# Performance work log

Hardware: AMD Instinct MI355X
Metric: run time of the kernel (lower is better)

Reference implementation:

```python
import jax, jax.numpy as jnp
import numpy as np

# sarModule stage: in=256, out=512, blocks=2, stride=2, patch_groups=4, mask_size=7
B, C_IN, H, W = 32, 256, 56, 56
C_OUT = 512
PLANES = C_OUT // 4   # Bottleneck inner width = planes // expansion = 128
G = 4                 # patch_groups
MS = 7                # mask_size
TEMP = 1.0            # gumbel-softmax temperature


def conv(x, w, stride=1, pad=0, groups=1):
    return jax.lax.conv_general_dilated(
        x, w, (stride, stride), [(pad, pad), (pad, pad)],
        feature_group_count=groups,
        dimension_numbers=('NCHW', 'OIHW', 'NCHW'))


def bn(x, g, b):
    # BatchNorm in inference form with running_mean=0, running_var=1 folded in
    return x * g[None, :, None, None] + b[None, :, None, None]


def avgpool3s2(x):
    # nn.AvgPool2d(3, stride=2, padding=1), count_include_pad=True
    s = jax.lax.reduce_window(x, 0.0, jax.lax.add, (1, 1, 3, 3), (1, 1, 2, 2),
                              [(0, 0), (0, 0), (1, 1), (1, 1)])
    return s / 9.0


def setup_inputs() -> dict:
    key = jax.random.key(0)
    ks = iter(jax.random.split(key, 64))

    def w(shape):
        fan_in = int(np.prod(shape[1:]))
        return jax.random.normal(next(ks), shape, jnp.float32) * np.float32((2.0 / fan_in) ** 0.5)

    ones = lambda n: jnp.ones((n,), jnp.float32)
    zeros = lambda n: jnp.zeros((n,), jnp.float32)

    x = jax.random.normal(next(ks), (B, C_IN, H, W), jnp.float32)
    u = jax.random.uniform(next(ks), (B, 2, G, MS, MS), jnp.float32, 1e-6, 1.0 - 1e-6)
    gumbel_noise = -jnp.log(-jnp.log(u))

    return dict(
        x=x, gumbel_noise=gumbel_noise,
        # base Bottleneck (256->512, stride 2, downsample = avgpool + 1x1 conv + bn)
        b_w1=w((PLANES, C_IN, 1, 1)), b_g1=ones(PLANES), b_b1=zeros(PLANES),
        b_w2=w((PLANES, PLANES, 3, 3)), b_g2=ones(PLANES), b_b2=zeros(PLANES),
        b_w3=w((C_OUT, PLANES, 1, 1)), b_g3=ones(C_OUT), b_b3=zeros(C_OUT),
        b_dw=w((C_OUT, C_IN, 1, 1)), b_dg=ones(C_OUT), b_db=zeros(C_OUT),
        # refine Bottleneck (256->512, stride 1, downsample = 1x1 conv + bn)
        r_w1=w((PLANES, C_IN, 1, 1)), r_g1=ones(PLANES), r_b1=zeros(PLANES),
        r_w2=w((PLANES, PLANES, 3, 3)), r_g2=ones(PLANES), r_b2=zeros(PLANES),
        r_w3=w((C_OUT, PLANES, 1, 1)), r_g3=ones(C_OUT), r_b3=zeros(C_OUT),
        r_dw=w((C_OUT, C_IN, 1, 1)), r_dg=ones(C_OUT), r_db=zeros(C_OUT),
        # maskGen: grouped 3x3 conv (512 -> 4*G), bn, pool, grouped 1x1 fc (4*G -> 2*G)
        m_w=w((4 * G, C_OUT // G, 3, 3)), m_g=ones(4 * G), m_b=zeros(4 * G),
        m_fcw=w((2 * G, 4, 1, 1)),
        m_fcb=jnp.concatenate([0.1 * ones(G), 5.0 * ones(G)]),  # bias init from maskGen
        # fusion Bottleneck (512->512, stride 2, downsample = avgpool only)
        f_w1=w((PLANES, C_OUT, 1, 1)), f_g1=ones(PLANES), f_b1=zeros(PLANES),
        f_w2=w((PLANES, PLANES, 3, 3)), f_g2=ones(PLANES), f_b2=zeros(PLANES),
        f_w3=w((C_OUT, PLANES, 1, 1)), f_g3=ones(C_OUT), f_b3=zeros(C_OUT),
    )


def reference(x, gumbel_noise,
              b_w1, b_g1, b_b1, b_w2, b_g2, b_b2, b_w3, b_g3, b_b3, b_dw, b_dg, b_db,
              r_w1, r_g1, r_b1, r_w2, r_g2, r_b2, r_w3, r_g3, r_b3, r_dw, r_dg, r_db,
              m_w, m_g, m_b, m_fcw, m_fcb,
              f_w1, f_g1, f_b1, f_w2, f_g2, f_b2, f_w3, f_g3, f_b3):
    # ---- base branch: Bottleneck stride 2, last_relu=False -> [B,512,28,28]
    o = jax.nn.relu(bn(conv(x, b_w1), b_g1, b_b1))
    o = jax.nn.relu(bn(conv(o, b_w2, stride=2, pad=1), b_g2, b_b2))
    o = bn(conv(o, b_w3), b_g3, b_b3)
    x_base = o + bn(conv(avgpool3s2(x), b_dw), b_dg, b_db)

    # ---- maskGen on x_base
    gmap = jax.nn.relu(bn(conv(x_base, m_w, pad=1, groups=G), m_g, m_b))      # [B,16,28,28]
    hb = x_base.shape[2] // MS                                                 # adaptive avgpool 28->7
    gmap = gmap.reshape(B, 4 * G, MS, hb, MS, hb).mean(axis=(3, 5))            # [B,16,7,7]
    logits = conv(gmap, m_fcw, groups=G) + m_fcb[None, :, None, None]          # [B,8,7,7]
    logits = logits.reshape(B, 2, G, MS, MS)                                   # view(B,2,groups,ms,ms)
    # hard gumbel-softmax over dim 1 with straight-through estimator
    y = jax.nn.softmax((logits + gumbel_noise) / TEMP, axis=1)
    hard = jax.nn.one_hot(jnp.argmax(y, axis=1), 2, axis=1, dtype=y.dtype)
    gates = hard + y - jax.lax.stop_gradient(y)
    mask = gates[:, 1]                                                         # [B,G,7,7]

    # nearest-upsample mask x8 and expand across each channel group
    mask_up = jnp.repeat(jnp.repeat(mask, H // MS, axis=-2), W // MS, axis=-1) # [B,G,56,56]
    mask_full = jnp.broadcast_to(mask_up[:, :, None], (B, G, C_OUT // G, H, W)).reshape(B, C_OUT, H, W)

    # ---- refine branch: Bottleneck stride 1, output gated by mask, last_relu=False
    o = jax.nn.relu(bn(conv(x, r_w1), r_g1, r_b1))
    o = jax.nn.relu(bn(conv(o, r_w2, pad=1), r_g2, r_b2))
    o = bn(conv(o, r_w3), r_g3, r_b3) * mask_full
    x_refine = o + bn(conv(x, r_dw), r_dg, r_db)                               # [B,512,56,56]

    # ---- fuse: bilinear upsample base to refine resolution (align_corners=False)
    x_base_up = jax.image.resize(x_base, (B, C_OUT, H, W), 'bilinear')
    fused = jax.nn.relu(x_base_up + x_refine)

    # ---- fusion Bottleneck: stride 2, downsample = avgpool only, last_relu=True
    o = jax.nn.relu(bn(conv(fused, f_w1), f_g1, f_b1))
    o = jax.nn.relu(bn(conv(o, f_w2, stride=2, pad=1), f_g2, f_b2))
    o = bn(conv(o, f_w3), f_g3, f_b3)
    out = jax.nn.relu(o + avgpool3s2(fused))                                   # [B,512,28,28]
    return out, mask
```

## Files before the change

### kernel.cpp

```cpp
#include <hip/hip_runtime.h>
#include <cstdint>

#define BB   32
#define CINX 256
#define HH   56
#define WW   56
#define HWX  3136
#define CO   512
#define PL   128
#define HP   28
#define WP   28
#define HWP  784
#define NG   4
#define MSZ  7

typedef unsigned short ushortT;
typedef unsigned int   uint32;
typedef __attribute__((ext_vector_type(8))) short short8;
typedef __attribute__((ext_vector_type(4))) float f32x4;

__device__ __forceinline__ ushortT f2bf(float f){
  uint32 u = __float_as_uint(f);
  u = (u + 0x7fffu + ((u >> 16) & 1u)) >> 16;
  return (ushortT)u;
}
__device__ __forceinline__ float bf2f(ushortT u){
  return __uint_as_float(((uint32)u) << 16);
}
__device__ __forceinline__ void split2(float v, ushortT& h, ushortT& lo){
  h = f2bf(v);
  lo = f2bf(v - bf2f(h));
}
__device__ __forceinline__ uint32 packu(ushortT a, ushortT b){
  return (uint32)a | ((uint32)b << 16);
}

typedef __attribute__((address_space(1))) const void g_void;
typedef __attribute__((address_space(3))) void l_void;
__device__ __forceinline__ void glds16(const ushortT* g, ushortT* l){
  __builtin_amdgcn_global_load_lds((g_void*)g, (l_void*)l, 16, 0, 0);
}

__device__ __forceinline__ void wsplit(float v, ushortT* dh, ushortT* dl, size_t i){
  ushortT h, lo; split2(v, h, lo); dh[i] = h; dl[i] = lo;
}

__global__ __launch_bounds__(256) void prep_w(
  const float* __restrict__ b_w1, const float* __restrict__ b_g1,
  const float* __restrict__ b_w2, const float* __restrict__ b_g2,
  const float* __restrict__ b_w3, const float* __restrict__ b_g3,
  const float* __restrict__ b_dw, const float* __restrict__ b_dg,
  const float* __restrict__ r_w1, const float* __restrict__ r_g1,
  const float* __restrict__ r_w2, const float* __restrict__ r_g2,
  const float* __restrict__ r_w3, const float* __restrict__ r_g3,
  const float* __restrict__ r_dw, const float* __restrict__ r_dg,
  const float* __restrict__ f_w1, const float* __restrict__ f_g1,
  const float* __restrict__ f_w2, const float* __restrict__ f_g2,
  const float* __restrict__ f_w3, const float* __restrict__ f_g3,
  const float* __restrict__ b_b1, const float* __restrict__ r_b1,
  ushortT* __restrict__ dh, ushortT* __restrict__ dl,
  ushortT* __restrict__ zp, float* __restrict__ biasC)
{
  const int idx = blockIdx.x*256 + threadIdx.x;
  switch (blockIdx.y){
    case 0: {
      if (idx >= 32768) return; int m = idx >> 8;
      wsplit(b_w1[idx]*b_g1[m], dh, dl, (size_t)0 + idx); } break;
    case 3: {
      if (idx >= 32768) return; int m = idx >> 8;
      wsplit(r_w1[idx]*r_g1[m], dh, dl, 32768 + (size_t)idx); } break;
    case 1: {
      if (idx >= 147456) return; int m = idx / 1152; int k = idx - m*1152;
      int tap = k >> 7, c = k & 127;
      wsplit(b_w2[((size_t)(m*128 + c))*9 + tap]*b_g2[m], dh, dl, 65536 + (size_t)idx); } break;
    case 2: {
      if (idx >= 196608) return; int m = idx / 384; int k = idx - m*384;
      float v = (k < 128) ? b_w3[m*128 + k]*b_g3[m] : b_dw[m*256 + (k-128)]*b_dg[m];
      wsplit(v, dh, dl, 212992 + (size_t)idx); } break;
    case 4: {
      if (idx >= 147456) return; int m = idx / 1152; int k = idx - m*1152;
      int tap = k >> 7, c = k & 127;
      wsplit(r_w2[((size_t)(m*128 + c))*9 + tap]*r_g2[m], dh, dl, 409600 + (size_t)idx); } break;
    case 5: {
      if (idx >= 196608) return; int m = idx / 384; int k = idx - m*384;
      float v = (k < 128) ? r_w3[m*128 + k]*r_g3[m] : r_dw[m*256 + (k-128)]*r_dg[m];
      wsplit(v, dh, dl, 557056 + (size_t)idx); } break;
    case 6: {
      if (idx >= 65536) return; int m = idx >> 9;
      wsplit(f_w1[idx]*f_g1[m], dh, dl, 753664 + (size_t)idx); } break;
    case 7: {
      if (idx >= 147456) return; int m = idx / 1152; int k = idx - m*1152;
      int tap = k >> 7, c = k & 127;
      wsplit(f_w2[((size_t)(m*128 + c))*9 + tap]*f_g2[m], dh, dl, 819200 + (size_t)idx); } break;
    case 8: {
      if (idx >= 65536) return; int m = idx >> 7;
      wsplit(f_w3[idx]*f_g3[m], dh, dl, 966656 + (size_t)idx); } break;
    case 9: {
      if (idx < 64) zp[idx] = 0;
      if (idx < 128) biasC[idx] = b_b1[idx];
      else if (idx < 256) biasC[idx] = r_b1[idx-128];
    } break;
  }
}

__global__ __launch_bounds__(256) void k_avgpool_x(const float* __restrict__ x, float* __restrict__ out){
  int idx = blockIdx.x*256 + threadIdx.x;
  if (idx >= BB*CINX*HWP) return;
  int p = idx % HWP; int bc = idx / HWP;
  int ox = p % WP, oy = p / WP;
  const float* src = x + (size_t)bc*HWX;
  float s = 0.f;
  #pragma unroll
  for (int dy=0; dy<3; dy++){
    int yy = 2*oy-1+dy;
    if ((unsigned)yy >= HH) continue;
    #pragma unroll
    for (int dx=0; dx<3; dx++){
      int xx = 2*ox-1+dx;
      if ((unsigned)xx >= WW) continue;
      s += src[yy*WW + xx];
    }
  }
  out[idx] = s * (1.f/9.f);
}

__global__ __launch_bounds__(256) void prep_p(const float* __restrict__ t,
    ushortT* __restrict__ ph_, ushortT* __restrict__ pl_){
  __shared__ float s[16][17];
  const int p0 = blockIdx.x*16, c0 = blockIdx.y*16, bz = blockIdx.z;
  const int ci = threadIdx.x >> 4, pi = threadIdx.x & 15;
  s[ci][pi] = t[((size_t)bz*CINX + c0 + ci)*HWP + p0 + pi];
  __syncthreads();
  const int pr = threadIdx.x >> 4, cj = threadIdx.x & 15;
  float v = s[cj][pr];
  ushortT h, lo; split2(v, h, lo);
  size_t o = ((size_t)bz*HWP + p0 + pr)*CINX + c0 + cj;
  ph_[o] = h; pl_[o] = lo;
}

__global__ __launch_bounds__(256) void prep_x2(const float* __restrict__ x,
    ushortT* __restrict__ xh, ushortT* __restrict__ xl){
  __shared__ float s[16][17];
  const int p0 = blockIdx.x*16, c0 = blockIdx.y*16, bz = blockIdx.z;
  const int ci = threadIdx.x >> 4, pi = threadIdx.x & 15;
  s[ci][pi] = x[((size_t)bz*CINX + c0 + ci)*HWX + p0 + pi];
  __syncthreads();
  const int pr = threadIdx.x >> 4, cj = threadIdx.x & 15;
  float v = s[cj][pr];
  ushortT h, lo; split2(v, h, lo);
  size_t o = ((size_t)bz*HWX + p0 + pr)*CINX + c0 + cj;
  xh[o] = h; xl[o] = lo;
}

__global__ __launch_bounds__(256) void k_poolf(const ushortT* __restrict__ fzh,
    const ushortT* __restrict__ fzl, float* __restrict__ pf){
  const int p = blockIdx.x, bz = blockIdx.y;
  const int oy = p / WP, ox = p - oy*WP;
  const int c = threadIdx.x*2;
  float s0 = 0.f, s1 = 0.f;
  #pragma unroll
  for (int dy=0; dy<3; dy++){
    const int iy = 2*oy - 1 + dy;
    if ((unsigned)iy >= (unsigned)HH) continue;
    #pragma unroll
    for (int dx=0; dx<3; dx++){
      const int ix = 2*ox - 1 + dx;
      if ((unsigned)ix >= (unsigned)WW) continue;
      const size_t fi = ((size_t)bz*HWX + (size_t)(iy*WW + ix))*CO + c;
      uint32 hh = *(const uint32*)(fzh + fi);
      uint32 ll = *(const uint32*)(fzl + fi);
      s0 += bf2f((ushortT)(hh & 0xffff)) + bf2f((ushortT)(ll & 0xffff));
      s1 += bf2f((ushortT)(hh >> 16))    + bf2f((ushortT)(ll >> 16));
    }
  }
  const size_t o = ((size_t)bz*HWP + p)*CO + c;
  pf[o]   = s0 * (1.f/9.f);
  pf[o+1] = s1 * (1.f/9.f);
}

template<int KIND,int EPI,int S1F,int MT,int DBUF,int SWAP,int STRIDE,int PAD,
         int HIN,int WIN,int WOUT,int NOUT,int C1,int C2,int BSTR1,int MTOT,int KTOT>
__global__ __launch_bounds__(MT*2)
void gemm_bf3(const ushortT* __restrict__ wph, const ushortT* __restrict__ wpl,
              const ushortT* __restrict__ s1h, const ushortT* __restrict__ s1l,
              const ushortT* __restrict__ s2h, const ushortT* __restrict__ s2l,
              const float* __restrict__ xf32,
              const float* __restrict__ bias1, const float* __restrict__ bias2,
              const float* __restrict__ maskf, const float* __restrict__ xbase,
              const ushortT* __restrict__ zp,
              ushortT* __restrict__ oh, ushortT* __restrict__ ol,
              float* __restrict__ of32)
{
  constexpr int NW = MT/32;
  constexpr int BCALLS = 8/NW;
  constexpr bool GATHER1 = (KIND==0 && S1F==1);
  constexpr int BUFSZ = MT*64 + 8192;
  __shared__ ushortT smem[BUFSZ*(DBUF+1)];

  const int tid = threadIdx.x;
  const int nt = SWAP ? blockIdx.y : blockIdx.x;
  const int mt = SWAP ? blockIdx.x : blockIdx.y;
  const int bz = blockIdx.z;
  const int l  = tid & 63, w = tid >> 6;
  const int wm = w >> 1, wn = w & 1;

  size_t a_src[2]; int a_dst[2];
  #pragma unroll
  for (int c=0;c<2;c++){
    int s = (w*2 + c)*64 + l;
    int row = s >> 2, slotm = s & 3;
    int logical = slotm ^ ((row >> 1) & 3);
    a_src[c] = (size_t)(mt*MT + row)*KTOT + logical*8;
    a_dst[c] = (w*2 + c)*512;
  }

  int b_dst[2]; size_t b_base1[2], b_base2[2]; int b_klane[2];
  int b_oy[2], b_ox[2]; bool b_ok[2]; float b_mv[2];
  #pragma unroll
  for (int c=0;c<BCALLS;c++){
    int s = (w*BCALLS + c)*64 + l;
    int row = s >> 2, slotm = s & 3;
    int logical = slotm ^ ((row >> 1) & 3);
    b_klane[c] = logical*8;
    b_dst[c] = (w*BCALLS + c)*512;
    int ngr = nt*128 + row;
    b_ok[c] = (ngr < NOUT);
    int oyv = ngr / WOUT, oxv = ngr - (ngr / WOUT)*WOUT;
    b_oy[c] = oyv; b_ox[c] = oxv;
    b_base1[c] = ((size_t)bz*NOUT + ngr)*BSTR1 + b_klane[c];
    b_base2[c] = ((size_t)bz*NOUT + ngr)*C2 + b_klane[c];
    b_mv[c] = 1.f;
    if (KIND == 3)
      b_mv[c] = b_ok[c] ? maskf[((size_t)(bz*NG + mt)*MSZ + (oyv>>3))*MSZ + (oxv>>3)] : 0.f;
  }

  const int sr = tid >> 1;
  const int hp = tid & 1;
  const int swz = (sr >> 1) & 3;
  const int lws0 = sr*32 + ((2*hp) ^ swz)*8;
  const int lws1 = sr*32 + ((2*hp + 1) ^ swz)*8;
  const int ng = nt*128 + sr;

  f32x4 acc[4][4];
  f32x4 zf = {0.f,0.f,0.f,0.f};
  #pragma unroll
  for (int i=0;i<4;i++)
    #pragma unroll
    for (int j=0;j<4;j++) acc[i][j] = zf;

  auto stagef = [&](int ks, ushortT* AHb, ushortT* ALb, ushortT* BHb, ushortT* BLb){
    const int k0 = ks*32;
    #pragma unroll
    for (int c=0;c<2;c++){
      glds16(wph + a_src[c] + k0, AHb + a_dst[c]);
      glds16(wpl + a_src[c] + k0, ALb + a_dst[c]);
    }
    if constexpr (GATHER1){
      if (tid < 256){
        uint4 b0 = make_uint4(0,0,0,0), b1v = b0, b2v = b0, b3v = b0;
        if (ng < NOUT){
          size_t fbase = ((size_t)bz*C1 + k0 + hp*16)*(size_t)NOUT + ng;
          ushortT h[16], lo[16];
          #pragma unroll
          for (int e=0;e<16;e++){ split2(xf32[fbase + (size_t)e*NOUT], h[e], lo[e]); }
          b0  = make_uint4(packu(h[0],h[1]),  packu(h[2],h[3]),  packu(h[4],h[5]),  packu(h[6],h[7]));
          b1v = make_uint4(packu(h[8],h[9]),  packu(h[10],h[11]),packu(h[12],h[13]),packu(h[14],h[15]));
          b2v = make_uint4(packu(lo[0],lo[1]),packu(lo[2],lo[3]),packu(lo[4],lo[5]),packu(lo[6],lo[7]));
          b3v = make_uint4(packu(lo[8],lo[9]),packu(lo[10],lo[11]),packu(lo[12],lo[13]),packu(lo[14],lo[15]));
        }
        *(uint4*)(BHb + lws0) = b0;  *(uint4*)(BHb + lws1) = b1v;
        *(uint4*)(BLb + lws0) = b2v; *(uint4*)(BLb + lws1) = b3v;
      }
    } else {
      #pragma unroll
      for (int c=0;c<BCALLS;c++){
        const ushortT *sh, *sl;
        if constexpr (KIND == 0){
          bool ok = b_ok[c];
          size_t off = b_base1[c] + k0;
          sh = ok ? s1h + off : zp;  sl = ok ? s1l + off : zp;
        } else if constexpr (KIND == 1){
          const int tap = k0 >> 7;
          const int cb  = (k0 & 127);
          const int dy = tap/3, dx = tap - 3*(tap/3);
          int iy = b_oy[c]*STRIDE + dy - PAD;
          int ix = b_ox[c]*STRIDE + dx - PAD;
          bool ok = b_ok[c] && (unsigned)iy < (unsigned)HIN && (unsigned)ix < (unsigned)WIN;
          size_t off = ((size_t)bz*(HIN*WIN) + (size_t)(iy*WIN + ix))*BSTR1 + cb + b_klane[c];
          sh = ok ? s1h + off : zp;  sl = ok ? s1l + off : zp;
        } else {
          if (k0 < C1){
            bool ok = b_ok[c] && (KIND != 3 || b_mv[c] != 0.f);
            size_t off = b_base1[c] + k0;
            sh = ok ? s1h + off : zp;  sl = ok ? s1l + off : zp;
          } else {
            bool ok = b_ok[c];
            size_t off = b_base2[c] + (k0 - C1);
            sh = ok ? s2h + off : zp;  sl = ok ? s2l + off : zp;
          }
        }
        glds16(sh, BHb + b_dst[c]);
        glds16(sl, BLb + b_dst[c]);
      }
    }
  };

  auto computef = [&](const ushortT* AHb, const ushortT* ALb,
                      const ushortT* BHb, const ushortT* BLb){
    short8 bh[4], bl[4];
    #pragma unroll
    for (int nf=0; nf<4; nf++){
      const int rr = wn*64 + nf*16 + (l & 15);
      const int ph = (l >> 4) ^ ((rr >> 1) & 3);
      bh[nf] = *(const short8*)(BHb + rr*32 + ph*8);
      bl[nf] = *(const short8*)(BLb + rr*32 + ph*8);
    }
    #pragma unroll
    for (int mf=0; mf<4; mf++){
      const int rr = wm*64 + mf*16 + (l & 15);
      const int ph = (l >> 4) ^ ((rr >> 1) & 3);
      short8 ah = *(const short8*)(AHb + rr*32 + ph*8);
      short8 al = *(const short8*)(ALb + rr*32 + ph*8);
      #pragma unroll
      for (int nf=0; nf<4; nf++)
        acc[mf][nf] = __builtin_amdgcn_mfma_f32_16x16x32_bf16(ah, bh[nf], acc[mf][nf], 0,0,0);
      #pragma unroll
      for (int nf=0; nf<4; nf++)
        acc[mf][nf] = __builtin_amdgcn_mfma_f32_16x16x32_bf16(ah, bl[nf], acc[mf][nf], 0,0,0);
      #pragma unroll
      for (int nf=0; nf<4; nf++)
        acc[mf][nf] = __builtin_amdgcn_mfma_f32_16x16x32_bf16(al, bh[nf], acc[mf][nf], 0,0,0);
    }
  };

  const int NK = KTOT / 32;
  if constexpr (DBUF == 0){
    ushortT* AH  = smem;
    ushortT* AL  = smem + MT*32;
    ushortT* BHs = smem + MT*64;
    ushortT* BLs = smem + MT*64 + 4096;
    for (int ks=0; ks<NK; ks++){
      stagef(ks, AH, AL, BHs, BLs);
      __syncthreads();
      computef(AH, AL, BHs, BLs);
      __syncthreads();
    }
  } else {
    stagef(0, smem, smem + MT*32, smem + MT*64, smem + MT*64 + 4096);
    __syncthreads();
    for (int ks=0; ks<NK; ks++){
      ushortT* cb = smem + (ks & 1)*BUFSZ;
      ushortT* nb = smem + ((ks & 1) ^ 1)*BUFSZ;
      if (ks + 1 < NK)
        stagef(ks + 1, nb, nb + MT*32, nb + MT*64, nb + MT*64 + 4096);
      computef(cb, cb + MT*32, cb + MT*64, cb + MT*64 + 4096);
      __syncthreads();
    }
  }

  const int mb0 = mt*MT + wm*64;
  const int nb0 = nt*128 + wn*64;

  #pragma unroll
  for (int nf=0; nf<4; nf++){
    const int n = nb0 + nf*16 + (l & 15);
    if (n >= NOUT) continue;
    if constexpr (EPI == 0){
      const size_t ob = ((size_t)bz*NOUT + n)*MTOT;
      #pragma unroll
      for (int mf=0; mf<4; mf++){
        const int m0 = mb0 + mf*16 + (l>>4)*4;
        ushort4 hq, lq; ushortT h0, l0; float v;
        v = fmaxf(acc[mf][nf][0] + bias1[m0+0], 0.f); split2(v,h0,l0); hq.x=h0; lq.x=l0;
        v = fmaxf(acc[mf][nf][1] + bias1[m0+1], 0.f); split2(v,h0,l0); hq.y=h0; lq.y=l0;
        v = fmaxf(acc[mf][nf][2] + bias1[m0+2], 0.f); split2(v,h0,l0); hq.z=h0; lq.z=l0;
        v = fmaxf(acc[mf][nf][3] + bias1[m0+3], 0.f); split2(v,h0,l0); hq.w=h0; lq.w=l0;
        *(ushort4*)(oh + ob + m0) = hq;
        *(ushort4*)(ol + ob + m0) = lq;
      }
    } else if constexpr (EPI == 1){
      #pragma unroll
      for (int mf=0; mf<4; mf++){
        const int m0 = mb0 + mf*16 + (l>>4)*4;
        #pragma unroll
        for (int r=0;r<4;r++){
          const int m = m0 + r;
          of32[((size_t)bz*MTOT + m)*NOUT + n] = acc[mf][nf][r] + bias1[m] + bias2[m];
        }
      }
    } else if constexpr (EPI == 2){
      const int y = n / WOUT, x = n - (n / WOUT)*WOUT;
      const int grpw = (mt*MT + wm*64) >> 7;
      const float mvv = maskf[((size_t)(bz*NG + grpw)*MSZ + (y>>3))*MSZ + (x>>3)];
      const int iy = y >> 1, ix = x >> 1;
      int yA,yB,xA,xB; float wyA,wyB,wxA,wxB;
      if (y & 1){ yA=iy; wyA=0.75f; yB=(iy+1<HP)?iy+1:HP-1; wyB=0.25f; }
      else      { yA=(iy>0)?iy-1:0; wyA=0.25f; yB=iy; wyB=0.75f; }
      if (x & 1){ xA=ix; wxA=0.75f; xB=(ix+1<WP)?ix+1:WP-1; wxB=0.25f; }
      else      { xA=(ix>0)?ix-1:0; wxA=0.25f; xB=ix; wxB=0.75f; }
      const size_t ob = ((size_t)bz*NOUT + n)*MTOT;
      #pragma unroll
      for (int mf=0; mf<4; mf++){
        const int m0 = mb0 + mf*16 + (l>>4)*4;
        ushort4 hq, lq;
        #pragma unroll
        for (int r=0;r<4;r++){
          const int m = m0 + r;
          const float* xb = xbase + ((size_t)bz*MTOT + m)*HWP;
          float up = wyA*(wxA*xb[yA*WP+xA] + wxB*xb[yA*WP+xB])
                   + wyB*(wxA*xb[yB*WP+xA] + wxB*xb[yB*WP+xB]);
          float v = fmaxf(acc[mf][nf][r] + up + mvv*bias1[m] + bias2[m], 0.f);
          ushortT h0, l0; split2(v, h0, l0);
          if      (r==0){hq.x=h0;lq.x=l0;}
          else if (r==1){hq.y=h0;lq.y=l0;}
          else if (r==2){hq.z=h0;lq.z=l0;}
          else          {hq.w=h0;lq.w=l0;}
        }
        *(ushort4*)(oh + ob + m0) = hq;
        *(ushort4*)(ol + ob + m0) = lq;
      }
    } else {
      const float* pfrow = xbase + ((size_t)bz*NOUT + n)*MTOT;
      #pragma unroll
      for (int mf=0; mf<4; mf++){
        const int m0 = mb0 + mf*16 + (l>>4)*4;
        const float4 pv = *(const float4*)(pfrow + m0);
        of32[((size_t)bz*MTOT + m0+0)*NOUT + n] = fmaxf(acc[mf][nf][0] + bias1[m0+0] + pv.x, 0.f);
        of32[((size_t)bz*MTOT + m0+1)*NOUT + n] = fmaxf(acc[mf][nf][1] + bias1[m0+1] + pv.y, 0.f);
        of32[((size_t)bz*MTOT + m0+2)*NOUT + n] = fmaxf(acc[mf][nf][2] + bias1[m0+2] + pv.z, 0.f);
        of32[((size_t)bz*MTOT + m0+3)*NOUT + n] = fmaxf(acc[mf][nf][3] + bias1[m0+3] + pv.w, 0.f);
      }
    }
  }
}

#define GM_LDSW 9216
__global__ __launch_bounds__(256) void k_gmap2(const float* __restrict__ xbase,
    const float* __restrict__ mw, const float* __restrict__ mg, const float* __restrict__ mb,
    float* __restrict__ gmap){
  __shared__ float wsh[GM_LDSW];
  __shared__ float red[16][2][4][16];
  const int tile = blockIdx.x, b = blockIdx.y;
  const int tid = threadIdx.x;
  const int pl = tid & 15, cs = tid >> 4;
  const int p = tile*16 + pl;
  const int oy = p / WP, ox = p - oy*WP;
  int toff[9];
  #pragma unroll
  for (int tap=0; tap<9; tap++){
    int dy = tap/3, dx = tap - 3*dy;
    int yy = oy + dy - 1, xx = ox + dx - 1;
    toff[tap] = ((unsigned)yy < (unsigned)HP && (unsigned)xx < (unsigned)WP) ? (yy*WP + xx) : -1;
  }
  float acc[2][4] = {{0.f,0.f,0.f,0.f},{0.f,0.f,0.f,0.f}};
  for (int pass=0; pass<2; pass++){
    __syncthreads();
    for (int i = tid; i < GM_LDSW; i += 256){
      int ocl = i & 3, tap = (i >> 2) % 9, c_rel = i / 36;
      int cg = pass*256 + c_rel;
      int g = cg >> 7;
      int oc = g*4 + ocl;
      wsh[i] = mw[((size_t)(oc*128 + (cg & 127)))*9 + tap] * mg[oc];
    }
    __syncthreads();
    const float* xb = xbase + ((size_t)b*CO + pass*256 + cs*16)*HWP;
    for (int cl=0; cl<16; cl++){
      const float* xc = xb + (size_t)cl*HWP;
      const float* wr = &wsh[(cs*16 + cl)*36];
      #pragma unroll
      for (int tap=0; tap<9; tap++){
        if (toff[tap] < 0) continue;
        float v = xc[toff[tap]];
        f32x4 w4 = *(const f32x4*)(wr + tap*4);
        acc[pass][0] += v*w4[0];
        acc[pass][1] += v*w4[1];
        acc[pass][2] += v*w4[2];
        acc[pass][3] += v*w4[3];
      }
    }
  }
  #pragma unroll
  for (int pp=0; pp<2; pp++)
    #pragma unroll
    for (int o=0; o<4; o++)
      red[cs][pp][o][pl] = acc[pp][o];
  __syncthreads();
  const int oc = tid >> 4;
  const int g = oc >> 2, ocl = oc & 3, pg = g >> 1, cs0 = (g & 1)*8;
  float s = 0.f;
  #pragma unroll
  for (int t=0; t<8; t++) s += red[cs0 + t][pg][ocl][pl];
  s = fmaxf(s + mb[oc], 0.f);
  gmap[((size_t)b*16 + oc)*HWP + p] = s;
}

__global__ __launch_bounds__(256) void k_gpool(const float* __restrict__ gmap, float* __restrict__ gpool){
  int idx = blockIdx.x*256 + threadIdx.x;
  if (idx >= BB*16*49) return;
  int q = idx % 49; int t = idx / 49; int ch = t % 16; int b = t / 16;
  int my = q/7, mx = q%7;
  const float* src = gmap + ((size_t)b*16 + ch)*HWP;
  float s = 0.f;
  #pragma unroll
  for (int yb=0;yb<4;yb++)
    #pragma unroll
    for (int xb=0;xb<4;xb++)
      s += src[(my*4+yb)*WP + (mx*4+xb)];
  gpool[idx] = s * (1.f/16.f);
}

__global__ __launch_bounds__(256) void k_mask(const float* __restrict__ gpool, const float* __restrict__ fcw,
    const float* __restrict__ fcb, const float* __restrict__ gum,
    float* __restrict__ maskf, float* __restrict__ mout){
  int idx = blockIdx.x*256 + threadIdx.x;
  if (idx >= BB*NG*49) return;
  int q = idx % 49; int t = idx / 49; int g = t % NG; int b = t / NG;
  float lgt[2];
  #pragma unroll
  for (int cls=0; cls<2; cls++){
    int c = cls*NG + g;
    int gc = c >> 1;
    float s = fcb[c];
    #pragma unroll
    for (int k=0;k<4;k++)
      s += fcw[c*4+k] * gpool[((size_t)b*16 + gc*4 + k)*49 + q];
    s += gum[(((size_t)b*2 + cls)*NG + g)*49 + q];
    lgt[cls] = s;
  }
  float m = (lgt[1] > lgt[0]) ? 1.f : 0.f;
  maskf[idx] = m;
  mout[idx] = m;
}

extern "C" void kernel_launch(void* const* d_in, const int* in_sizes, int n_in,
                              void* d_out, int out_size, void* d_ws, size_t ws_size,
                              hipStream_t stream){
  const float* x    = (const float*)d_in[0];
  const float* gum  = (const float*)d_in[1];
  const float* b_w1 = (const float*)d_in[2];
  const float* b_g1 = (const float*)d_in[3];
  const float* b_b1 = (const float*)d_in[4];
  const float* b_w2 = (const float*)d_in[5];
  const float* b_g2 = (const float*)d_in[6];
  const float* b_b2 = (const float*)d_in[7];
  const float* b_w3 = (const float*)d_in[8];
  const float* b_g3 = (const float*)d_in[9];
  const float* b_b3 = (const float*)d_in[10];
  const float* b_dw = (const float*)d_in[11];
  const float* b_dg = (const float*)d_in[12];
  const float* b_db = (const float*)d_in[13];
  const float* r_w1 = (const float*)d_in[14];
  const float* r_g1 = (const float*)d_in[15];
  const float* r_b1 = (const float*)d_in[16];
  const float* r_w2 = (const float*)d_in[17];
  const float* r_g2 = (const float*)d_in[18];
  const float* r_b2 = (const float*)d_in[19];
  const float* r_w3 = (const float*)d_in[20];
  const float* r_g3 = (const float*)d_in[21];
  const float* r_b3 = (const float*)d_in[22];
  const float* r_dw = (const float*)d_in[23];
  const float* r_dg = (const float*)d_in[24];
  const float* r_db = (const float*)d_in[25];
  const float* m_w  = (const float*)d_in[26];
  const float* m_g  = (const float*)d_in[27];
  const float* m_b  = (const float*)d_in[28];
  const float* m_fcw= (const float*)d_in[29];
  const float* m_fcb= (const float*)d_in[30];
  const float* f_w1 = (const float*)d_in[31];
  const float* f_g1 = (const float*)d_in[32];
  const float* f_b1 = (const float*)d_in[33];
  const float* f_w2 = (const float*)d_in[34];
  const float* f_g2 = (const float*)d_in[35];
  const float* f_b2 = (const float*)d_in[36];
  const float* f_w3 = (const float*)d_in[37];
  const float* f_g3 = (const float*)d_in[38];
  const float* f_b3 = (const float*)d_in[39];

  char* ws = (char*)d_ws;
  constexpr size_t O_WPH  = 0;
  constexpr size_t O_WPL  = 2064384;
  constexpr size_t O_CH   = 4128768;
  constexpr size_t O_DH   = 55508992;
  constexpr size_t O_DL   = 61931520;
  constexpr size_t O_EH   = 68354048;
  constexpr size_t O_EL   = 94044160;
  constexpr size_t O_PF   = O_EH;
  constexpr size_t O_XB   = 119734272;
  constexpr size_t O_GMAP = 171114496;
  constexpr size_t O_GPOOL= 172720128;
  constexpr size_t O_MASK = 172820480;
  constexpr size_t O_FH   = 172845568;
  constexpr size_t O_PH   = 172845568;
  constexpr size_t O_PL   = 185690624;
  constexpr size_t O_FL   = 275606016;
  constexpr size_t O_ZP   = 378366464;
  constexpr size_t O_BIASC= 378366592;

  ushortT* WPH = (ushortT*)(ws + O_WPH);
  ushortT* WPL = (ushortT*)(ws + O_WPL);
  ushortT* MGH = (ushortT*)(ws + O_CH);
  ushortT* XH  = (ushortT*)(ws + O_CH);
  ushortT* F1H = (ushortT*)(ws + O_CH);
  ushortT* F1L = (ushortT*)(ws + O_CH + 25690112);
  ushortT* DHp = (ushortT*)(ws + O_DH);
  ushortT* DLp = (ushortT*)(ws + O_DL);
  ushortT* EHp = (ushortT*)(ws + O_EH);
  ushortT* ELp = (ushortT*)(ws + O_EL);
  float*   PF  = (float*)(ws + O_PF);
  float*   XB  = (float*)(ws + O_XB);
  float*   PTMP= (float*)(ws + O_XB);
  ushortT* PHp = (ushortT*)(ws + O_PH);
  ushortT* PLp = (ushortT*)(ws + O_PL);
  ushortT* FHp = (ushortT*)(ws + O_FH);
  ushortT* FLp = (ushortT*)(ws + O_FL);
  float*   GMAP = (float*)(ws + O_GMAP);
  float*   GPOOL= (float*)(ws + O_GPOOL);
  float*   MASKF= (float*)(ws + O_MASK);
  ushortT* ZP  = (ushortT*)(ws + O_ZP);
  float*   BIASC = (float*)(ws + O_BIASC);
  (void)ws_size;

  float* outp = (float*)d_out;
  float* mout = outp + (size_t)BB*CO*HWP;
  ushortT* dout_u = (ushortT*)d_out;

  dim3 blk(256), blk2(512);
  const ushortT* nu = nullptr; const float* nf_ = nullptr;
  ushortT* nuo = nullptr; float* nfo = nullptr;

  prep_w<<<dim3(768, 10), blk, 0, stream>>>(b_w1,b_g1,b_w2,b_g2,b_w3,b_g3,b_dw,b_dg,
      r_w1,r_g1,r_w2,r_g2,r_w3,r_g3,r_dw,r_dg,f_w1,f_g1,f_w2,f_g2,f_w3,f_g3,
      b_b1, r_b1, WPH, WPL, ZP, BIASC);
  k_avgpool_x<<<dim3((BB*CINX*HWP+255)/256), blk, 0, stream>>>(x, PTMP);
  prep_p<<<dim3(49, 16, BB), blk, 0, stream>>>(PTMP, PHp, PLp);

  gemm_bf3<0,0,1,256,0,0, 1,0,56,56,56,3136, 256,0,256, 256,256><<<dim3(25,1,BB), blk2, 0, stream>>>(
      WPH+0, WPL+0, nu, nu, nu, nu, x, BIASC, nf_, nf_, nf_, ZP, MGH, dout_u, nfo);
  gemm_bf3<1,0,0,128,1,0, 2,1,56,56,28,784, 128,0,256, 128,1152><<<dim3(7,1,BB), blk, 0, stream>>>(
      WPH+65536, WPL+65536, MGH, dout_u, nu, nu, nf_, b_b2, nf_, nf_, nf_, ZP, DHp, DLp, nfo);
  gemm_bf3<2,1,0,256,0,0, 1,0,28,28,28,784, 128,256,128, 512,384><<<dim3(7,2,BB), blk2, 0, stream>>>(
      WPH+212992, WPL+212992, DHp, DLp, PHp, PLp, nf_, b_b3, b_db, nf_, nf_, ZP, nuo, nuo, XB);

  k_gmap2<<<dim3(49, BB), blk, 0, stream>>>(XB, m_w, m_g, m_b, GMAP);
  k_gpool<<<dim3(98), blk, 0, stream>>>(GMAP, GPOOL);
  k_mask<<<dim3(25), blk, 0, stream>>>(GPOOL, m_fcw, m_fcb, gum, MASKF, mout);

  gemm_bf3<1,0,0,128,1,0, 1,1,56,56,56,3136, 128,0,256, 128,1152><<<dim3(25,1,BB), blk, 0, stream>>>(
      WPH+409600, WPL+409600, MGH+128, dout_u+128, nu, nu, nf_, r_b2, nf_, nf_, nf_, ZP, EHp, ELp, nfo);

  prep_x2<<<dim3(196, 16, BB), blk, 0, stream>>>(x, XH, dout_u);

  gemm_bf3<3,2,0,128,1,1, 1,0,56,56,56,3136, 128,256,128, 512,384><<<dim3(4,25,BB), blk, 0, stream>>>(
      WPH+557056, WPL+557056, EHp, ELp, XH, dout_u, nf_, r_b3, r_db, MASKF, XB, ZP, FHp, FLp, nfo);

  k_poolf<<<dim3(HWP, BB), blk, 0, stream>>>(FHp, FLp, PF);

  gemm_bf3<0,0,0,128,1,0, 1,0,56,56,56,3136, 512,0,512, 128,512><<<dim3(25,1,BB), blk, 0, stream>>>(
      WPH+753664, WPL+753664, FHp, FLp, nu, nu, nf_, f_b1, nf_, nf_, nf_, ZP, F1H, F1L, nfo);
  gemm_bf3<1,0,0,128,1,0, 2,1,56,56,28,784, 128,0,128, 128,1152><<<dim3(7,1,BB), blk, 0, stream>>>(
      WPH+819200, WPL+819200, F1H, F1L, nu, nu, nf_, f_b2, nf_, nf_, nf_, ZP, DHp, DLp, nfo);
  gemm_bf3<0,3,0,256,0,0, 1,0,28,28,28,784, 128,0,128, 512,128><<<dim3(7,2,BB), blk2, 0, stream>>>(
      WPH+966656, WPL+966656, DHp, DLp, nu, nu, nf_, f_b3, nf_, nf_, PF, ZP, nuo, nuo, outp);
}
```

Before: 1.074 ms.

## Remap GEMM blocks for XCD-aware L2 locality and fuse avgpool into prep

```diff
diff --git a/kernel.cpp b/kernel.cpp
--- a/kernel.cpp
+++ b/kernel.cpp
@@ -103,33 +103,29 @@
   }
 }
 
-__global__ __launch_bounds__(256) void k_avgpool_x(const float* __restrict__ x, float* __restrict__ out){
-  int idx = blockIdx.x*256 + threadIdx.x;
-  if (idx >= BB*CINX*HWP) return;
-  int p = idx % HWP; int bc = idx / HWP;
-  int ox = p % WP, oy = p / WP;
-  const float* src = x + (size_t)bc*HWX;
-  float s = 0.f;
-  #pragma unroll
-  for (int dy=0; dy<3; dy++){
-    int yy = 2*oy-1+dy;
-    if ((unsigned)yy >= HH) continue;
-    #pragma unroll
-    for (int dx=0; dx<3; dx++){
-      int xx = 2*ox-1+dx;
-      if ((unsigned)xx >= WW) continue;
-      s += src[yy*WW + xx];
-    }
-  }
-  out[idx] = s * (1.f/9.f);
-}
-
-__global__ __launch_bounds__(256) void prep_p(const float* __restrict__ t,
+__global__ __launch_bounds__(256) void k_pool2(const float* __restrict__ x,
     ushortT* __restrict__ ph_, ushortT* __restrict__ pl_){
   __shared__ float s[16][17];
   const int p0 = blockIdx.x*16, c0 = blockIdx.y*16, bz = blockIdx.z;
   const int ci = threadIdx.x >> 4, pi = threadIdx.x & 15;
-  s[ci][pi] = t[((size_t)bz*CINX + c0 + ci)*HWP + p0 + pi];
+  {
+    const int p = p0 + pi;
+    const int oy = p / WP, ox = p - oy*WP;
+    const float* src = x + ((size_t)bz*CINX + c0 + ci)*HWX;
+    float sum = 0.f;
+    #pragma unroll
+    for (int dy=0; dy<3; dy++){
+      int yy = 2*oy-1+dy;
+      if ((unsigned)yy >= HH) continue;
+      #pragma unroll
+      for (int dx=0; dx<3; dx++){
+        int xx = 2*ox-1+dx;
+        if ((unsigned)xx >= WW) continue;
+        sum += src[yy*WW + xx];
+      }
+    }
+    s[ci][pi] = sum * (1.f/9.f);
+  }
   __syncthreads();
   const int pr = threadIdx.x >> 4, cj = threadIdx.x & 15;
   float v = s[cj][pr];
@@ -178,7 +174,7 @@
   pf[o+1] = s1 * (1.f/9.f);
 }
 
-template<int KIND,int EPI,int S1F,int MT,int DBUF,int SWAP,int STRIDE,int PAD,
+template<int KIND,int EPI,int S1F,int MT,int DBUF,int SWAP,int GX,int GY,int STRIDE,int PAD,
          int HIN,int WIN,int WOUT,int NOUT,int C1,int C2,int BSTR1,int MTOT,int KTOT>
 __global__ __launch_bounds__(MT*2)
 void gemm_bf3(const ushortT* __restrict__ wph, const ushortT* __restrict__ wpl,
@@ -195,12 +191,20 @@
   constexpr int BCALLS = 8/NW;
   constexpr bool GATHER1 = (KIND==0 && S1F==1);
   constexpr int BUFSZ = MT*64 + 8192;
+  constexpr int T = GX*GY*BB;
+  static_assert(T % 8 == 0, "grid not divisible by 8 XCDs");
+  constexpr int QX = T/8;
   __shared__ ushortT smem[BUFSZ*(DBUF+1)];
 
   const int tid = threadIdx.x;
-  const int nt = SWAP ? blockIdx.y : blockIdx.x;
-  const int mt = SWAP ? blockIdx.x : blockIdx.y;
-  const int bz = blockIdx.z;
+  const int lin = blockIdx.x;
+  const int virt = (lin & 7)*QX + (lin >> 3);
+  const int vx = virt % GX;
+  const int vrest = virt / GX;
+  const int vy = vrest % GY;
+  const int bz = vrest / GY;
+  const int nt = SWAP ? vy : vx;
+  const int mt = SWAP ? vx : vy;
   const int l  = tid & 63, w = tid >> 6;
   const int wm = w >> 1, wn = w & 1;
 
@@ -608,7 +612,6 @@
   ushortT* ELp = (ushortT*)(ws + O_EL);
   float*   PF  = (float*)(ws + O_PF);
   float*   XB  = (float*)(ws + O_XB);
-  float*   PTMP= (float*)(ws + O_XB);
   ushortT* PHp = (ushortT*)(ws + O_PH);
   ushortT* PLp = (ushortT*)(ws + O_PL);
   ushortT* FHp = (ushortT*)(ws + O_FH);
@@ -631,34 +634,33 @@
   prep_w<<<dim3(768, 10), blk, 0, stream>>>(b_w1,b_g1,b_w2,b_g2,b_w3,b_g3,b_dw,b_dg,
       r_w1,r_g1,r_w2,r_g2,r_w3,r_g3,r_dw,r_dg,f_w1,f_g1,f_w2,f_g2,f_w3,f_g3,
       b_b1, r_b1, WPH, WPL, ZP, BIASC);
-  k_avgpool_x<<<dim3((BB*CINX*HWP+255)/256), blk, 0, stream>>>(x, PTMP);
-  prep_p<<<dim3(49, 16, BB), blk, 0, stream>>>(PTMP, PHp, PLp);
-
-  gemm_bf3<0,0,1,256,0,0, 1,0,56,56,56,3136, 256,0,256, 256,256><<<dim3(25,1,BB), blk2, 0, stream>>>(
+  k_pool2<<<dim3(49, 16, BB), blk, 0, stream>>>(x, PHp, PLp);
+
+  gemm_bf3<0,0,1,256,0,0, 25,1, 1,0,56,56,56,3136, 256,0,256, 256,256><<<dim3(800), blk2, 0, stream>>>(
       WPH+0, WPL+0, nu, nu, nu, nu, x, BIASC, nf_, nf_, nf_, ZP, MGH, dout_u, nfo);
-  gemm_bf3<1,0,0,128,1,0, 2,1,56,56,28,784, 128,0,256, 128,1152><<<dim3(7,1,BB), blk, 0, stream>>>(
+  gemm_bf3<1,0,0,128,1,0, 7,1, 2,1,56,56,28,784, 128,0,256, 128,1152><<<dim3(224), blk, 0, stream>>>(
       WPH+65536, WPL+65536, MGH, dout_u, nu, nu, nf_, b_b2, nf_, nf_, nf_, ZP, DHp, DLp, nfo);
-  gemm_bf3<2,1,0,256,0,0, 1,0,28,28,28,784, 128,256,128, 512,384><<<dim3(7,2,BB), blk2, 0, stream>>>(
+  gemm_bf3<2,1,0,256,0,0, 7,2, 1,0,28,28,28,784, 128,256,128, 512,384><<<dim3(448), blk2, 0, stream>>>(
       WPH+212992, WPL+212992, DHp, DLp, PHp, PLp, nf_, b_b3, b_db, nf_, nf_, ZP, nuo, nuo, XB);
 
   k_gmap2<<<dim3(49, BB), blk, 0, stream>>>(XB, m_w, m_g, m_b, GMAP);
   k_gpool<<<dim3(98), blk, 0, stream>>>(GMAP, GPOOL);
   k_mask<<<dim3(25), blk, 0, stream>>>(GPOOL, m_fcw, m_fcb, gum, MASKF, mout);
 
-  gemm_bf3<1,0,0,128,1,0, 1,1,56,56,56,3136, 128,0,256, 128,1152><<<dim3(25,1,BB), blk, 0, stream>>>(
+  gemm_bf3<1,0,0,128,1,0, 25,1, 1,1,56,56,56,3136, 128,0,256, 128,1152><<<dim3(800), blk, 0, stream>>>(
       WPH+409600, WPL+409600, MGH+128, dout_u+128, nu, nu, nf_, r_b2, nf_, nf_, nf_, ZP, EHp, ELp, nfo);
 
   prep_x2<<<dim3(196, 16, BB), blk, 0, stream>>>(x, XH, dout_u);
 
-  gemm_bf3<3,2,0,128,1,1, 1,0,56,56,56,3136, 128,256,128, 512,384><<<dim3(4,25,BB), blk, 0, stream>>>(
+  gemm_bf3<3,2,0,128,1,1, 4,25, 1,0,56,56,56,3136, 128,256,128, 512,384><<<dim3(3200), blk, 0, stream>>>(
       WPH+557056, WPL+557056, EHp, ELp, XH, dout_u, nf_, r_b3, r_db, MASKF, XB, ZP, FHp, FLp, nfo);
 
   k_poolf<<<dim3(HWP, BB), blk, 0, stream>>>(FHp, FLp, PF);
 
-  gemm_bf3<0,0,0,128,1,0, 1,0,56,56,56,3136, 512,0,512, 128,512><<<dim3(25,1,BB), blk, 0, stream>>>(
+  gemm_bf3<0,0,0,128,1,0, 25,1, 1,0,56,56,56,3136, 512,0,512, 128,512><<<dim3(800), blk, 0, stream>>>(
       WPH+753664, WPL+753664, FHp, FLp, nu, nu, nf_, f_b1, nf_, nf_, nf_, ZP, F1H, F1L, nfo);
-  gemm_bf3<1,0,0,128,1,0, 2,1,56,56,28,784, 128,0,128, 128,1152><<<dim3(7,1,BB), blk, 0, stream>>>(
+  gemm_bf3<1,0,0,128,1,0, 7,1, 2,1,56,56,28,784, 128,0,128, 128,1152><<<dim3(224), blk, 0, stream>>>(
       WPH+819200, WPL+819200, F1H, F1L, nu, nu, nf_, f_b2, nf_, nf_, nf_, ZP, DHp, DLp, nfo);
-  gemm_bf3<0,3,0,256,0,0, 1,0,28,28,28,784, 128,0,128, 512,128><<<dim3(7,2,BB), blk2, 0, stream>>>(
+  gemm_bf3<0,3,0,256,0,0, 7,2, 1,0,28,28,28,784, 128,0,128, 512,128><<<dim3(448), blk2, 0, stream>>>(
       WPH+966656, WPL+966656, DHp, DLp, nu, nu, nf_, f_b3, nf_, nf_, PF, ZP, nuo, nuo, outp);
 }
```

After: 1.055 ms. Within noise of the previous version (-1.8%).
